# Optimization experiments

Hardware: AMD Instinct MI355X
Metric: run time of the kernel (lower is better)

The kernel has to match this reference:

```python
import jax, jax.numpy as jnp
import numpy as np

D_MODEL = 768
NUM_HEADS = 12
HEAD_DIM = D_MODEL // NUM_HEADS


def setup_inputs() -> dict:
    key = jax.random.key(0)
    ks = jax.random.split(key, 9)
    B, S = 2, 2048
    s = 1.0 / np.sqrt(D_MODEL)
    x = jax.random.normal(ks[0], (B, S, D_MODEL), dtype=jnp.float32)
    Wq = jax.random.normal(ks[1], (D_MODEL, D_MODEL), dtype=jnp.float32) * s
    Wk = jax.random.normal(ks[2], (D_MODEL, D_MODEL), dtype=jnp.float32) * s
    Wv = jax.random.normal(ks[3], (D_MODEL, D_MODEL), dtype=jnp.float32) * s
    Wo = jax.random.normal(ks[4], (D_MODEL, D_MODEL), dtype=jnp.float32) * s
    bq = jax.random.normal(ks[5], (D_MODEL,), dtype=jnp.float32) * 0.01
    bk = jax.random.normal(ks[6], (D_MODEL,), dtype=jnp.float32) * 0.01
    bv = jax.random.normal(ks[7], (D_MODEL,), dtype=jnp.float32) * 0.01
    bo = jax.random.normal(ks[8], (D_MODEL,), dtype=jnp.float32) * 0.01
    return {"x": x, "Wq": Wq, "bq": bq, "Wk": Wk, "bk": bk,
            "Wv": Wv, "bv": bv, "Wo": Wo, "bo": bo}


def reference(x, Wq, bq, Wk, bk, Wv, bv, Wo, bo):
    B, S, _ = x.shape
    # projections; reshape to [B, H, S, Dh]
    def split_heads(t):
        return t.reshape(B, S, NUM_HEADS, HEAD_DIM).transpose(0, 2, 1, 3)
    q = split_heads(x @ Wq + bq)
    k = split_heads(x @ Wk + bk)
    v = split_heads(x @ Wv + bv)
    scale = 1.0 / np.sqrt(HEAD_DIM)
    scores = jnp.einsum("bhqd,bhkd->bhqk", q, k) * scale  # [B,H,S,S]
    attn = jax.nn.softmax(scores, axis=-1)
    # dropout p=0.0 (eval) -> identity
    ctx = jnp.einsum("bhqk,bhkd->bhqd", attn, v)
    ctx = ctx.transpose(0, 2, 1, 3).reshape(B, S, D_MODEL)
    return ctx @ Wo + bo
```

## Files before the change

### kernel.cpp

```cpp
#include <hip/hip_runtime.h>
#include <hip/hip_bf16.h>
#include <hip/hip_fp16.h>

#define D_MODEL 768
#define NHEADS  12
#define HD      64
#define BATCH   2
#define SEQ     2048
#define NTOK    (BATCH*SEQ)
#define NX      ((size_t)NTOK * D_MODEL)
#define NW      ((size_t)D_MODEL * D_MODEL)
#define NBH     (BATCH*NHEADS)
#define SC_LOG2 0.18033688f

typedef __attribute__((ext_vector_type(8))) short    short8;
typedef __attribute__((ext_vector_type(8))) _Float16 half8;
typedef __attribute__((ext_vector_type(2))) __fp16   fp16x2;
typedef __attribute__((ext_vector_type(4))) float    f32x4;

__device__ __forceinline__ float bf2f(short s) {
    union { unsigned u; float f; } c;
    c.u = ((unsigned)(unsigned short)s) << 16;
    return c.f;
}
__device__ __forceinline__ short f2bf(float f) {
    __hip_bfloat16 h = __float2bfloat16(f);
    return *(short*)&h;
}

#ifdef __has_builtin
#if __has_builtin(__builtin_amdgcn_global_load_lds)
#define HAS_GLD 1
#endif
#if __has_builtin(__builtin_amdgcn_exp2f)
#define EXP2(x) __builtin_amdgcn_exp2f(x)
#else
#define EXP2(x) exp2f(x)
#endif
#if __has_builtin(__builtin_amdgcn_cvt_pkrtz)
#define HAS_PKRTZ 1
#endif
#else
#define EXP2(x) exp2f(x)
#endif
#ifdef HAS_GLD
#define GLD16(gp, lp) __builtin_amdgcn_global_load_lds( \
    (const __attribute__((address_space(1))) void*)(gp), \
    (__attribute__((address_space(3))) void*)(lp), 16, 0, 0)
#endif

#ifdef HAS_PKRTZ
#define PKF16(a, b) __builtin_amdgcn_cvt_pkrtz((a), (b))
#else
#define PKF16(a, b) ((fp16x2){ (__fp16)(a), (__fp16)(b) })
#endif

__global__ __launch_bounds__(256) void fused_conv(
        const void* __restrict__ xin,
        const void* __restrict__ w0, const void* __restrict__ w1,
        const void* __restrict__ w2, const void* __restrict__ w3,
        const void* __restrict__ b0, const void* __restrict__ b1,
        const void* __restrict__ b2, const void* __restrict__ b3,
        short* __restrict__ xc, short* __restrict__ wt,
        short* __restrict__ bc, int* __restrict__ flag)
{
    __shared__ int red[256];
    __shared__ float T[64][65];
    const int tid = threadIdx.x;
    const int F = blockIdx.x;

    {
        const short* xs = (const short*)xin;
        int maxe = 0;
#pragma unroll
        for (int u = 0; u < 16; ++u) {
            int e = ((unsigned short)xs[tid * 16 + u] >> 7) & 0xFF;
            maxe = max(maxe, e);
        }
        red[tid] = maxe;
        __syncthreads();
        for (int s = 128; s > 0; s >>= 1) {
            if (tid < s) red[tid] = max(red[tid], red[tid + s]);
            __syncthreads();
        }
    }
    const bool isf = (red[0] > 140);

    if (F < 3072) {
        const int i = F * 256 + tid;
        if (isf) {
            float4 f = ((const float4*)xin)[i];
            short4 o = { f2bf(f.x), f2bf(f.y), f2bf(f.z), f2bf(f.w) };
            ((short4*)xc)[i] = o;
        } else {
            ((short4*)xc)[i] = ((const short4*)xin)[i];
        }
    } else if (F < 3648) {
        const int G = F - 3072;
        const int z = G / 144, rr = G % 144;
        const int k0 = (rr % 12) * 64, n0 = (rr / 12) * 64;
        const void* src = (z == 0) ? w0 : (z == 1) ? w1 : (z == 2) ? w2 : w3;
        const float sc = (z == 0) ? SC_LOG2 : 1.0f;
        const int la = tid & 15, lb = tid >> 4;
#pragma unroll
        for (int u = 0; u < 4; ++u) {
            const int kr = (lb & 3) + 4 * u + 16 * (lb >> 2);
            if (isf) {
                float4 f = *(const float4*)((const float*)src + (size_t)(k0 + kr) * D_MODEL + n0 + la * 4);
                T[kr][la*4+0] = f.x; T[kr][la*4+1] = f.y; T[kr][la*4+2] = f.z; T[kr][la*4+3] = f.w;
            } else {
                short4 s = *(const short4*)((const short*)src + (size_t)(k0 + kr) * D_MODEL + n0 + la * 4);
                T[kr][la*4+0] = bf2f(s.x); T[kr][la*4+1] = bf2f(s.y);
                T[kr][la*4+2] = bf2f(s.z); T[kr][la*4+3] = bf2f(s.w);
            }
        }
        __syncthreads();
#pragma unroll
        for (int u = 0; u < 4; ++u) {
            const int nr = (lb & 3) + 4 * u + 16 * (lb >> 2);
            short4 o = { f2bf(T[la*4+0][nr] * sc), f2bf(T[la*4+1][nr] * sc),
                         f2bf(T[la*4+2][nr] * sc), f2bf(T[la*4+3][nr] * sc) };
            *(short4*)(wt + (size_t)z * NW + (size_t)(n0 + nr) * D_MODEL + k0 + la * 4) = o;
        }
    } else {
        if (tid == 0) *flag = isf ? 1 : 0;
        const void* srcs[4] = { b0, b1, b2, b3 };
        for (int z = 0; z < 4; ++z) {
            const float sc = (z == 0) ? SC_LOG2 : 1.0f;
            for (int i = tid; i < D_MODEL; i += 256) {
                float v = isf ? ((const float*)srcs[z])[i] : bf2f(((const short*)srcs[z])[i]);
                bc[z * D_MODEL + i] = f2bf(v * sc);
            }
        }
    }
}

__global__ __launch_bounds__(256) void qkv_gemm(const short* __restrict__ X,
                                                const short* __restrict__ Wt,
                                                const short* __restrict__ bias,
                                                short* __restrict__ qb,
                                                short* __restrict__ kb,
                                                _Float16* __restrict__ Vt)
{
    __shared__ __align__(16) char shbuf[24576];
    short* Als = (short*)shbuf;
    short* Bls = (short*)(shbuf + 8192);
    _Float16* T = (_Float16*)shbuf;

    const int tid = threadIdx.x;
    const int wave = tid >> 6, lane = tid & 63;
    const int quad = lane >> 4, l16 = lane & 15;
    const int wm = wave & 1, wn = wave >> 1;
    const int m0 = blockIdx.x * 64;
    const int ng = blockIdx.y * 128;

    f32x4 acc[2][4];
#pragma unroll
    for (int nt = 0; nt < 4; ++nt) {
        const float bv = bf2f(bias[ng + wn*64 + nt*16 + l16]);
#pragma unroll
        for (int mt = 0; mt < 2; ++mt) acc[mt][nt] = (f32x4){bv, bv, bv, bv};
    }

    const int row = tid >> 2, ch = (tid & 3) * 8;
#ifdef HAS_GLD
#define QSTAGE(buf, k0) do { \
        GLD16(X  + (size_t)(m0 + row)      * D_MODEL + (k0) + ch, &Als[(buf)*2048 + tid*8]); \
        GLD16(Wt + (size_t)(ng + row)      * D_MODEL + (k0) + ch, &Bls[(buf)*4096 + tid*8]); \
        GLD16(Wt + (size_t)(ng + 64 + row) * D_MODEL + (k0) + ch, &Bls[(buf)*4096 + 2048 + tid*8]); \
    } while (0)
#else
#define QSTAGE(buf, k0) do { \
        short8 r0 = *(const short8*)(X  + (size_t)(m0 + row)      * D_MODEL + (k0) + ch); \
        short8 r2 = *(const short8*)(Wt + (size_t)(ng + row)      * D_MODEL + (k0) + ch); \
        short8 r3 = *(const short8*)(Wt + (size_t)(ng + 64 + row) * D_MODEL + (k0) + ch); \
        *(short8*)&Als[(buf)*2048 + tid*8] = r0; \
        *(short8*)&Bls[(buf)*4096 + tid*8] = r2; \
        *(short8*)&Bls[(buf)*4096 + 2048 + tid*8] = r3; \
    } while (0)
#endif

    QSTAGE(0, 0);
    __syncthreads();

    for (int ks = 0; ks < 24; ++ks) {
        const int cur = ks & 1;
        if (ks + 1 < 24) QSTAGE(cur ^ 1, (ks + 1) * 32);

        short8 a[2], b[4];
#pragma unroll
        for (int mt = 0; mt < 2; ++mt)
            a[mt] = *(const short8*)&Als[cur*2048 + (wm*32 + mt*16 + l16) * 32 + quad*8];
#pragma unroll
        for (int nt = 0; nt < 4; ++nt)
            b[nt] = *(const short8*)&Bls[cur*4096 + (wn*64 + nt*16 + l16) * 32 + quad*8];
#pragma unroll
        for (int mt = 0; mt < 2; ++mt)
#pragma unroll
        for (int nt = 0; nt < 4; ++nt)
            acc[mt][nt] = __builtin_amdgcn_mfma_f32_16x16x32_bf16(a[mt], b[nt], acc[mt][nt], 0, 0, 0);

        __syncthreads();
    }
#undef QSTAGE

    const int seg = blockIdx.y / 6;
    if (seg < 2) {
        short* out = seg ? kb : qb;
        const int nl = ng - seg * 768;
#pragma unroll
        for (int mt = 0; mt < 2; ++mt)
#pragma unroll
        for (int nt = 0; nt < 4; ++nt) {
            const int n = nl + wn*64 + nt*16 + l16;
#pragma unroll
            for (int r = 0; r < 4; ++r) {
                const int m = m0 + wm*32 + mt*16 + quad*4 + r;
                out[(size_t)m * D_MODEL + n] = f2bf(acc[mt][nt][r]);
            }
        }
    } else {
        const int batch = m0 >> 11, tokb = m0 & (SEQ - 1);
#pragma unroll
        for (int nt = 0; nt < 4; ++nt) {
            const int dim_l = wn*64 + nt*16 + l16;
#pragma unroll
            for (int mt = 0; mt < 2; ++mt) {
                const int tok_l = wm*32 + mt*16 + quad*4;
                union { _Float16 h4[4]; int2 v; } u;
#pragma unroll
                for (int r = 0; r < 4; ++r) u.h4[r] = (_Float16)acc[mt][nt][r];
                *(int2*)&T[dim_l * 72 + tok_l] = u.v;
            }
        }
        __syncthreads();
#pragma unroll
        for (int u = 0; u < 4; ++u) {
            const int slot = tid + u * 256;
            const int drow = slot >> 3, chk = slot & 7;
            int4 val = *(const int4*)&T[drow * 72 + chk * 8];
            const int dim_g = ng - 1536 + drow;
            const int h = dim_g >> 6, d = dim_g & 63;
            *(int4*)(Vt + ((size_t)(batch * NHEADS + h) * HD + d) * SEQ + tokb + chk*8) = val;
        }
    }
}

__global__ __launch_bounds__(256) void out_gemm(const short* __restrict__ X,
                                                const short* __restrict__ Wt,
                                                const short* __restrict__ bias,
                                                void* __restrict__ outv,
                                                const int* __restrict__ flag)
{
    __shared__ short Als[2][2048];
    __shared__ short Bls[2][2048];

    const int tid = threadIdx.x;
    const int wave = tid >> 6, lane = tid & 63;
    const int quad = lane >> 4, l16 = lane & 15;
    const int m0 = blockIdx.x * 64;
    const int n0 = blockIdx.y * 64;

    f32x4 acc[4];
#pragma unroll
    for (int nt = 0; nt < 4; ++nt) {
        const float bv = bf2f(bias[n0 + nt*16 + l16]);
        acc[nt] = (f32x4){bv, bv, bv, bv};
    }

    const int row = tid >> 2, ch = (tid & 3) * 8;
#ifdef HAS_GLD
#define OSTAGE(buf, k0) do { \
        GLD16(X  + (size_t)(m0 + row) * D_MODEL + (k0) + ch, &Als[buf][tid*8]); \
        GLD16(Wt + (size_t)(n0 + row) * D_MODEL + (k0) + ch, &Bls[buf][tid*8]); \
    } while (0)
#else
#define OSTAGE(buf, k0) do { \
        short8 r0 = *(const short8*)(X  + (size_t)(m0 + row) * D_MODEL + (k0) + ch); \
        short8 r1 = *(const short8*)(Wt + (size_t)(n0 + row) * D_MODEL + (k0) + ch); \
        *(short8*)&Als[buf][tid*8] = r0; \
        *(short8*)&Bls[buf][tid*8] = r1; \
    } while (0)
#endif

    OSTAGE(0, 0);
    __syncthreads();

    for (int ks = 0; ks < 24; ++ks) {
        const int cur = ks & 1;
        if (ks + 1 < 24) OSTAGE(cur ^ 1, (ks + 1) * 32);

        short8 a = *(const short8*)&Als[cur][(wave*16 + l16) * 32 + quad*8];
#pragma unroll
        for (int nt = 0; nt < 4; ++nt) {
            short8 b = *(const short8*)&Bls[cur][(nt*16 + l16) * 32 + quad*8];
            acc[nt] = __builtin_amdgcn_mfma_f32_16x16x32_bf16(a, b, acc[nt], 0, 0, 0);
        }
        __syncthreads();
    }
#undef OSTAGE

    const bool outf32 = (*flag != 0);
#pragma unroll
    for (int nt = 0; nt < 4; ++nt) {
        const int n = n0 + nt*16 + l16;
#pragma unroll
        for (int r = 0; r < 4; ++r) {
            const int m = m0 + wave*16 + quad*4 + r;
            const size_t idx = (size_t)m * D_MODEL + n;
            if (outf32) ((float*)outv)[idx] = acc[nt][r];
            else        ((short*)outv)[idx] = f2bf(acc[nt][r]);
        }
    }
}

__global__ __launch_bounds__(256, 6) void attn_mfma(const short* __restrict__ q,
                                                    const short* __restrict__ k,
                                                    const _Float16* __restrict__ Vt,
                                                    _Float16* __restrict__ Op,
                                                    float* __restrict__ mlp)
{
    __shared__ short    Kls[2][2048];
    __shared__ _Float16 Vls[3][2048];
    __shared__ _Float16 Pls[4][512];

    const int tid  = threadIdx.x;
    const int wave = tid >> 6, lane = tid & 63;
    const int quad = lane >> 4, l16 = lane & 15;

    const int F = blockIdx.x;
    const int xcd = F & 7, slot = F >> 3;
    const int bh = xcd * 3 + (slot >> 6);
    const int rem = slot & 63;
    const int q0 = (rem >> 1) * 64;
    const int sp = rem & 1;
    const int kb0 = sp * (SEQ / 2);
    const int b = bh / NHEADS, h = bh % NHEADS;
    const size_t bS = (size_t)b * SEQ;
    const int myq = q0 + wave * 16 + l16;

    short8 qf[2];
#pragma unroll
    for (int k0h = 0; k0h < 2; ++k0h)
        qf[k0h] = *(const short8*)(q + (bS + myq) * D_MODEL + h*HD + k0h*32 + quad*8);

    half8 ones;
#pragma unroll
    for (int j = 0; j < 8; ++j) ones[j] = (_Float16)1.0f;

    const int cK = tid >> 5, keyK = tid & 31;
    const int cV = tid >> 6, dimV = tid & 63;
    const short*    kgp = k  + (bS + kb0 + keyK) * D_MODEL + h*HD + cK*8;
    const _Float16* vgp = Vt + ((size_t)bh * HD + dimV) * SEQ + kb0 + cV*8;

#ifdef HAS_GLD
#define STAGE_K(buf, j0) GLD16(kgp + (size_t)(j0) * D_MODEL, &Kls[buf][tid*8])
#define STAGE_V(buf, j0) GLD16(vgp + (j0),                   &Vls[buf][tid*8])
#else
#define STAGE_K(buf, j0) do { \
        short8 a_ = *(const short8*)(kgp + (size_t)(j0) * D_MODEL); \
        *(short8*)&Kls[buf][tid*8] = a_; } while (0)
#define STAGE_V(buf, j0) do { \
        half8 c_ = *(const half8*)(vgp + (j0)); \
        *(half8*)&Vls[buf][tid*8] = c_; } while (0)
#endif

    float m_ = -1e30f;
    f32x4 lacc = (f32x4){0.f, 0.f, 0.f, 0.f};
    f32x4 o[4];
#pragma unroll
    for (int t = 0; t < 4; ++t) o[t] = (f32x4){0.f, 0.f, 0.f, 0.f};

    f32x4 sA[2], sB[2];

#define NT (SEQ / 2 / 32)

#define QK(S, KB) do { \
    S[0] = (f32x4){0.f,0.f,0.f,0.f}; S[1] = (f32x4){0.f,0.f,0.f,0.f}; \
    __builtin_amdgcn_s_setprio(1); \
    _Pragma("unroll") \
    for (int k0h = 0; k0h < 2; ++k0h) \
    _Pragma("unroll") \
    for (int t = 0; t < 2; ++t) { \
        short8 kf = *(const short8*)&Kls[KB][(k0h*4 + quad)*256 + (t*16 + l16)*8]; \
        S[t] = __builtin_amdgcn_mfma_f32_16x16x32_bf16(kf, qf[k0h], S[t], 0, 0, 0); \
    } \
    __builtin_amdgcn_s_setprio(0); \
} while (0)

#define BODY(JT, SCUR, SNXT) do { \
    if ((JT) + 2 < NT) { \
        STAGE_K(((JT) + 2) & 1, ((JT) + 2) * 32); \
        STAGE_V(((JT) + 2) % 3, ((JT) + 2) * 32); \
    } \
    if ((JT) + 1 < NT) QK(SNXT, ((JT) + 1) & 1); \
    { \
         \
        float mx = SCUR[0][0]; \
        _Pragma("unroll") \
        for (int t = 0; t < 2; ++t) \
        _Pragma("unroll") \
        for (int r = 0; r < 4; ++r) mx = fmaxf(mx, SCUR[t][r]); \
        if (__any(mx > m_ + 8.f)) { \
            _Pragma("unroll") \
            for (int d = 1; d < 64; d <<= 1) mx = fmaxf(mx, __shfl_xor(mx, d)); \
            const float mn = fmaxf(m_, mx); \
            const float al = EXP2(m_ - mn); \
            _Pragma("unroll") \
            for (int t = 0; t < 4; ++t) { \
                o[t][0] *= al; o[t][1] *= al; o[t][2] *= al; o[t][3] *= al; \
            } \
            lacc[0] *= al; \
            m_ = mn; \
        } \
         \
        _Pragma("unroll") \
        for (int t = 0; t < 2; ++t) { \
            union { fp16x2 h2[2]; int2 v; } u4; \
            u4.h2[0] = PKF16(EXP2(SCUR[t][0] - m_), EXP2(SCUR[t][1] - m_)); \
            u4.h2[1] = PKF16(EXP2(SCUR[t][2] - m_), EXP2(SCUR[t][3] - m_)); \
            const int c = 2*t + (quad >> 1); \
            *(int2*)&Pls[wave][c*128 + l16*8 + (quad & 1)*4] = u4.v; \
        } \
         \
        const int vb = (JT) % 3; \
        half8 pf = *(half8*)&Pls[wave][quad*128 + l16*8]; \
        __builtin_amdgcn_s_setprio(1); \
        lacc = __builtin_amdgcn_mfma_f32_16x16x32_f16(ones, pf, lacc, 0, 0, 0); \
        _Pragma("unroll") \
        for (int t = 0; t < 4; ++t) { \
            half8 vf = *(const half8*)&Vls[vb][quad*512 + (t*16 + l16)*8]; \
            o[t] = __builtin_amdgcn_mfma_f32_16x16x32_f16(vf, pf, o[t], 0, 0, 0); \
        } \
        __builtin_amdgcn_s_setprio(0); \
    } \
    __syncthreads(); \
} while (0)

    STAGE_K(0, 0); STAGE_V(0, 0);
    __syncthreads();
    STAGE_K(1, 32); STAGE_V(1, 32);
    QK(sA, 0);
    __syncthreads();

    for (int jt = 0; jt < NT; jt += 2) {
        BODY(jt,     sA, sB);
        BODY(jt + 1, sB, sA);
    }

    const float inv = 1.0f / lacc[0];
    const size_t prow = ((size_t)sp * (NBH * SEQ) + (size_t)bh * SEQ + myq);
    _Float16* orow = Op + prow * HD;
#pragma unroll
    for (int t = 0; t < 4; ++t) {
        union { _Float16 h4[4]; int2 v; } u4;
#pragma unroll
        for (int r = 0; r < 4; ++r) u4.h4[r] = (_Float16)(o[t][r] * inv);
        *(int2*)(orow + t*16 + quad*4) = u4.v;
    }
    if (quad == 0) {
        float2 mlv; mlv.x = m_; mlv.y = lacc[0];
        *(float2*)&mlp[prow * 2] = mlv;
    }
#undef BODY
#undef QK
#undef NT
#undef STAGE_K
#undef STAGE_V
}

__global__ __launch_bounds__(256) void attn_combine(const _Float16* __restrict__ Op,
                                                    const float* __restrict__ mlp,
                                                    short* __restrict__ ctx)
{
    const int gid = blockIdx.x * 256 + threadIdx.x;
    const int r = gid >> 3, seg = gid & 7;
    const float2 a  = *(const float2*)&mlp[(size_t)r * 2];
    const float2 c2 = *(const float2*)&mlp[((size_t)(NBH * SEQ) + r) * 2];
    const float M  = fmaxf(a.x, c2.x);
    const float w1 = EXP2(a.x - M) * a.y;
    const float w2 = EXP2(c2.x - M) * c2.y;
    const float inv = 1.0f / (w1 + w2);
    const half8 o1 = *(const half8*)&Op[(size_t)r * HD + seg * 8];
    const half8 o2 = *(const half8*)&Op[(size_t)(NBH * SEQ) * HD + (size_t)r * HD + seg * 8];
    union { short s[8]; int4 v; } u;
#pragma unroll
    for (int j = 0; j < 8; ++j)
        u.s[j] = f2bf((w1 * (float)o1[j] + w2 * (float)o2[j]) * inv);
    const int bh = r >> 11, qq = r & (SEQ - 1);
    const int bb = bh / NHEADS, hh = bh % NHEADS;
    *(int4*)&ctx[((size_t)(bb * SEQ + qq)) * D_MODEL + hh * HD + seg * 8] = u.v;
}

extern "C" void kernel_launch(void* const* d_in, const int* in_sizes, int n_in,
                              void* d_out, int out_size, void* d_ws, size_t ws_size,
                              hipStream_t stream)
{
    int* flag = (int*)d_ws;
    short* xc = (short*)((char*)d_ws + 64);
    short* Wt = xc + NX;
    short* bc = Wt + 4 * NW;
    short* qb = bc + 4 * D_MODEL;
    short* kb = qb + NX;
    _Float16* Vt = (_Float16*)(kb + NX);
    short* cb = (short*)(Vt + NX);
    _Float16* Op = (_Float16*)(cb + NX);
    float* mlp = (float*)(Op + (size_t)2 * NBH * SEQ * HD);

    fused_conv<<<3649, 256, 0, stream>>>(d_in[0],
                                         d_in[1], d_in[3], d_in[5], d_in[7],
                                         d_in[2], d_in[4], d_in[6], d_in[8],
                                         xc, Wt, bc, flag);

    qkv_gemm<<<dim3(NTOK/64, 2304/128), 256, 0, stream>>>(xc, Wt, bc, qb, kb, Vt);

    attn_mfma<<<1536, 256, 0, stream>>>(qb, kb, Vt, Op, mlp);

    attn_combine<<<1536, 256, 0, stream>>>(Op, mlp, cb);

    out_gemm<<<dim3(NTOK/64, D_MODEL/64), 256, 0, stream>>>(cb, Wt + 3*NW, bc + 3*D_MODEL, d_out, flag);
}
```

Before: 189.8 us.

## Enlarge attention tiles to 32 queries per wave and 64-key blocks

Result: slower. 195.9 us (+3.2%).

```diff
diff --git a/kernel.cpp b/kernel.cpp
--- a/kernel.cpp
+++ b/kernel.cpp
@@ -314,15 +314,15 @@
     }
 }
 
-__global__ __launch_bounds__(256, 6) void attn_mfma(const short* __restrict__ q,
+__global__ __launch_bounds__(256, 3) void attn_mfma(const short* __restrict__ q,
                                                     const short* __restrict__ k,
                                                     const _Float16* __restrict__ Vt,
                                                     _Float16* __restrict__ Op,
                                                     float* __restrict__ mlp)
 {
-    __shared__ short    Kls[2][2048];
-    __shared__ _Float16 Vls[3][2048];
-    __shared__ _Float16 Pls[4][512];
+    __shared__ __align__(16) short    Kls[2][4096];
+    __shared__ __align__(16) _Float16 Vls[2][4096];
+    __shared__ __align__(16) _Float16 Pls[4][2048];
 
     const int tid  = threadIdx.x;
     const int wave = tid >> 6, lane = tid & 63;
@@ -330,107 +330,135 @@
 
     const int F = blockIdx.x;
     const int xcd = F & 7, slot = F >> 3;
-    const int bh = xcd * 3 + (slot >> 6);
-    const int rem = slot & 63;
-    const int q0 = (rem >> 1) * 64;
+    const int bh = xcd * 3 + (slot >> 5);
+    const int rem = slot & 31;
+    const int q0 = (rem >> 1) * 128;
     const int sp = rem & 1;
     const int kb0 = sp * (SEQ / 2);
     const int b = bh / NHEADS, h = bh % NHEADS;
     const size_t bS = (size_t)b * SEQ;
-    const int myq = q0 + wave * 16 + l16;
-
-    short8 qf[2];
+
+    short8 qf[2][2];
+#pragma unroll
+    for (int col = 0; col < 2; ++col)
 #pragma unroll
     for (int k0h = 0; k0h < 2; ++k0h)
-        qf[k0h] = *(const short8*)(q + (bS + myq) * D_MODEL + h*HD + k0h*32 + quad*8);
+        qf[col][k0h] = *(const short8*)(q + (bS + q0 + wave*32 + col*16 + l16) * D_MODEL
+                                          + h*HD + k0h*32 + quad*8);
 
     half8 ones;
 #pragma unroll
     for (int j = 0; j < 8; ++j) ones[j] = (_Float16)1.0f;
 
-    const int cK = tid >> 5, keyK = tid & 31;
-    const int cV = tid >> 6, dimV = tid & 63;
-    const short*    kgp = k  + (bS + kb0 + keyK) * D_MODEL + h*HD + cK*8;
-    const _Float16* vgp = Vt + ((size_t)bh * HD + dimV) * SEQ + kb0 + cV*8;
+    const int cK0 = tid >> 6,       keyK0 = tid & 63;
+    const int cK1 = (tid + 256) >> 6, keyK1 = tid & 63;
+    const short* kgp0 = k + (bS + kb0 + keyK0) * D_MODEL + h*HD + cK0*8;
+    const short* kgp1 = k + (bS + kb0 + keyK1) * D_MODEL + h*HD + cK1*8;
+    const _Float16* vgp0 = Vt + ((size_t)bh * HD + keyK0) * SEQ + kb0 + cK0*8;
+    const _Float16* vgp1 = Vt + ((size_t)bh * HD + keyK1) * SEQ + kb0 + cK1*8;
 
 #ifdef HAS_GLD
-#define STAGE_K(buf, j0) GLD16(kgp + (size_t)(j0) * D_MODEL, &Kls[buf][tid*8])
-#define STAGE_V(buf, j0) GLD16(vgp + (j0),                   &Vls[buf][tid*8])
+#define STAGE_K(buf, j0) do { \
+        GLD16(kgp0 + (size_t)(j0) * D_MODEL, &Kls[buf][tid*8]); \
+        GLD16(kgp1 + (size_t)(j0) * D_MODEL, &Kls[buf][(tid+256)*8]); \
+    } while (0)
+#define STAGE_V(buf, j0) do { \
+        GLD16(vgp0 + (j0), &Vls[buf][tid*8]); \
+        GLD16(vgp1 + (j0), &Vls[buf][(tid+256)*8]); \
+    } while (0)
 #else
 #define STAGE_K(buf, j0) do { \
-        short8 a_ = *(const short8*)(kgp + (size_t)(j0) * D_MODEL); \
-        *(short8*)&Kls[buf][tid*8] = a_; } while (0)
+        short8 a_ = *(const short8*)(kgp0 + (size_t)(j0) * D_MODEL); \
+        short8 b_ = *(const short8*)(kgp1 + (size_t)(j0) * D_MODEL); \
+        *(short8*)&Kls[buf][tid*8] = a_;  *(short8*)&Kls[buf][(tid+256)*8] = b_; \
+    } while (0)
 #define STAGE_V(buf, j0) do { \
-        half8 c_ = *(const half8*)(vgp + (j0)); \
-        *(half8*)&Vls[buf][tid*8] = c_; } while (0)
+        half8 c_ = *(const half8*)(vgp0 + (j0)); \
+        half8 d_ = *(const half8*)(vgp1 + (j0)); \
+        *(half8*)&Vls[buf][tid*8] = c_;  *(half8*)&Vls[buf][(tid+256)*8] = d_; \
+    } while (0)
 #endif
 
     float m_ = -1e30f;
-    f32x4 lacc = (f32x4){0.f, 0.f, 0.f, 0.f};
-    f32x4 o[4];
-#pragma unroll
-    for (int t = 0; t < 4; ++t) o[t] = (f32x4){0.f, 0.f, 0.f, 0.f};
-
-    f32x4 sA[2], sB[2];
-
-#define NT (SEQ / 2 / 32)
+    f32x4 laccA = (f32x4){0.f,0.f,0.f,0.f}, laccB = (f32x4){0.f,0.f,0.f,0.f};
+    f32x4 o[4][2];
+#pragma unroll
+    for (int t = 0; t < 4; ++t) { o[t][0] = (f32x4){0.f,0.f,0.f,0.f}; o[t][1] = (f32x4){0.f,0.f,0.f,0.f}; }
+
+    f32x4 sA[4][2], sB[4][2];
+
+#define NT (SEQ / 2 / 64)
 
 #define QK(S, KB) do { \
-    S[0] = (f32x4){0.f,0.f,0.f,0.f}; S[1] = (f32x4){0.f,0.f,0.f,0.f}; \
+    _Pragma("unroll") \
+    for (int t = 0; t < 4; ++t) { S[t][0] = (f32x4){0.f,0.f,0.f,0.f}; S[t][1] = (f32x4){0.f,0.f,0.f,0.f}; } \
     __builtin_amdgcn_s_setprio(1); \
     _Pragma("unroll") \
     for (int k0h = 0; k0h < 2; ++k0h) \
     _Pragma("unroll") \
-    for (int t = 0; t < 2; ++t) { \
-        short8 kf = *(const short8*)&Kls[KB][(k0h*4 + quad)*256 + (t*16 + l16)*8]; \
-        S[t] = __builtin_amdgcn_mfma_f32_16x16x32_bf16(kf, qf[k0h], S[t], 0, 0, 0); \
+    for (int t = 0; t < 4; ++t) { \
+        short8 kf = *(const short8*)&Kls[KB][(k0h*4 + quad)*512 + (t*16 + l16)*8]; \
+        S[t][0] = __builtin_amdgcn_mfma_f32_16x16x32_bf16(kf, qf[0][k0h], S[t][0], 0, 0, 0); \
+        S[t][1] = __builtin_amdgcn_mfma_f32_16x16x32_bf16(kf, qf[1][k0h], S[t][1], 0, 0, 0); \
     } \
     __builtin_amdgcn_s_setprio(0); \
 } while (0)
 
 #define BODY(JT, SCUR, SNXT) do { \
-    if ((JT) + 2 < NT) { \
-        STAGE_K(((JT) + 2) & 1, ((JT) + 2) * 32); \
-        STAGE_V(((JT) + 2) % 3, ((JT) + 2) * 32); \
+    if ((JT) + 2 < NT) STAGE_K(((JT) + 2) & 1, ((JT) + 2) * 64); \
+    if ((JT) + 1 < NT) { \
+        STAGE_V(((JT) + 1) & 1, ((JT) + 1) * 64); \
+        QK(SNXT, ((JT) + 1) & 1); \
     } \
-    if ((JT) + 1 < NT) QK(SNXT, ((JT) + 1) & 1); \
     { \
          \
-        float mx = SCUR[0][0]; \
+        float mx = SCUR[0][0][0]; \
         _Pragma("unroll") \
-        for (int t = 0; t < 2; ++t) \
+        for (int t = 0; t < 4; ++t) \
         _Pragma("unroll") \
-        for (int r = 0; r < 4; ++r) mx = fmaxf(mx, SCUR[t][r]); \
+        for (int c = 0; c < 2; ++c) \
+        _Pragma("unroll") \
+        for (int r = 0; r < 4; ++r) mx = fmaxf(mx, SCUR[t][c][r]); \
         if (__any(mx > m_ + 8.f)) { \
             _Pragma("unroll") \
             for (int d = 1; d < 64; d <<= 1) mx = fmaxf(mx, __shfl_xor(mx, d)); \
             const float mn = fmaxf(m_, mx); \
             const float al = EXP2(m_ - mn); \
             _Pragma("unroll") \
-            for (int t = 0; t < 4; ++t) { \
-                o[t][0] *= al; o[t][1] *= al; o[t][2] *= al; o[t][3] *= al; \
+            for (int t = 0; t < 4; ++t) \
+            _Pragma("unroll") \
+            for (int c = 0; c < 2; ++c) { \
+                o[t][c][0] *= al; o[t][c][1] *= al; o[t][c][2] *= al; o[t][c][3] *= al; \
             } \
-            lacc[0] *= al; \
+            laccA[0] *= al; laccB[0] *= al; \
             m_ = mn; \
         } \
          \
         _Pragma("unroll") \
-        for (int t = 0; t < 2; ++t) { \
+        for (int t = 0; t < 4; ++t) \
+        _Pragma("unroll") \
+        for (int c = 0; c < 2; ++c) { \
             union { fp16x2 h2[2]; int2 v; } u4; \
-            u4.h2[0] = PKF16(EXP2(SCUR[t][0] - m_), EXP2(SCUR[t][1] - m_)); \
-            u4.h2[1] = PKF16(EXP2(SCUR[t][2] - m_), EXP2(SCUR[t][3] - m_)); \
-            const int c = 2*t + (quad >> 1); \
-            *(int2*)&Pls[wave][c*128 + l16*8 + (quad & 1)*4] = u4.v; \
+            u4.h2[0] = PKF16(EXP2(SCUR[t][c][0] - m_), EXP2(SCUR[t][c][1] - m_)); \
+            u4.h2[1] = PKF16(EXP2(SCUR[t][c][2] - m_), EXP2(SCUR[t][c][3] - m_)); \
+            const int kc = 2*t + (quad >> 1); \
+            *(int2*)&Pls[wave][c*1024 + kc*128 + l16*8 + (quad & 1)*4] = u4.v; \
         } \
          \
-        const int vb = (JT) % 3; \
-        half8 pf = *(half8*)&Pls[wave][quad*128 + l16*8]; \
+        const int vb = (JT) & 1; \
         __builtin_amdgcn_s_setprio(1); \
-        lacc = __builtin_amdgcn_mfma_f32_16x16x32_f16(ones, pf, lacc, 0, 0, 0); \
         _Pragma("unroll") \
-        for (int t = 0; t < 4; ++t) { \
-            half8 vf = *(const half8*)&Vls[vb][quad*512 + (t*16 + l16)*8]; \
-            o[t] = __builtin_amdgcn_mfma_f32_16x16x32_f16(vf, pf, o[t], 0, 0, 0); \
+        for (int k0h = 0; k0h < 2; ++k0h) { \
+            half8 pf0 = *(half8*)&Pls[wave][(k0h*4 + quad)*128 + l16*8]; \
+            half8 pf1 = *(half8*)&Pls[wave][1024 + (k0h*4 + quad)*128 + l16*8]; \
+            laccA = __builtin_amdgcn_mfma_f32_16x16x32_f16(ones, pf0, laccA, 0, 0, 0); \
+            laccB = __builtin_amdgcn_mfma_f32_16x16x32_f16(ones, pf1, laccB, 0, 0, 0); \
+            _Pragma("unroll") \
+            for (int t = 0; t < 4; ++t) { \
+                half8 vf = *(const half8*)&Vls[vb][(k0h*4 + quad)*512 + (t*16 + l16)*8]; \
+                o[t][0] = __builtin_amdgcn_mfma_f32_16x16x32_f16(vf, pf0, o[t][0], 0, 0, 0); \
+                o[t][1] = __builtin_amdgcn_mfma_f32_16x16x32_f16(vf, pf1, o[t][1], 0, 0, 0); \
+            } \
         } \
         __builtin_amdgcn_s_setprio(0); \
     } \
@@ -439,7 +467,7 @@
 
     STAGE_K(0, 0); STAGE_V(0, 0);
     __syncthreads();
-    STAGE_K(1, 32); STAGE_V(1, 32);
+    STAGE_K(1, 64);
     QK(sA, 0);
     __syncthreads();
 
@@ -448,19 +476,24 @@
         BODY(jt + 1, sB, sA);
     }
 
-    const float inv = 1.0f / lacc[0];
-    const size_t prow = ((size_t)sp * (NBH * SEQ) + (size_t)bh * SEQ + myq);
-    _Float16* orow = Op + prow * HD;
-#pragma unroll
-    for (int t = 0; t < 4; ++t) {
-        union { _Float16 h4[4]; int2 v; } u4;
-#pragma unroll
-        for (int r = 0; r < 4; ++r) u4.h4[r] = (_Float16)(o[t][r] * inv);
-        *(int2*)(orow + t*16 + quad*4) = u4.v;
-    }
-    if (quad == 0) {
-        float2 mlv; mlv.x = m_; mlv.y = lacc[0];
-        *(float2*)&mlp[prow * 2] = mlv;
+#pragma unroll
+    for (int col = 0; col < 2; ++col) {
+        const f32x4 la = col ? laccB : laccA;
+        const float inv = 1.0f / la[0];
+        const int myq = q0 + wave*32 + col*16 + l16;
+        const size_t prow = ((size_t)sp * (NBH * SEQ) + (size_t)bh * SEQ + myq);
+        _Float16* orow = Op + prow * HD;
+#pragma unroll
+        for (int t = 0; t < 4; ++t) {
+            union { _Float16 h4[4]; int2 v; } u4;
+#pragma unroll
+            for (int r = 0; r < 4; ++r) u4.h4[r] = (_Float16)(o[t][col][r] * inv);
+            *(int2*)(orow + t*16 + quad*4) = u4.v;
+        }
+        if (quad == 0) {
+            float2 mlv; mlv.x = m_; mlv.y = la[0];
+            *(float2*)&mlp[prow * 2] = mlv;
+        }
     }
 #undef BODY
 #undef QK
@@ -514,7 +547,7 @@
 
     qkv_gemm<<<dim3(NTOK/64, 2304/128), 256, 0, stream>>>(xc, Wt, bc, qb, kb, Vt);
 
-    attn_mfma<<<1536, 256, 0, stream>>>(qb, kb, Vt, Op, mlp);
+    attn_mfma<<<768, 256, 0, stream>>>(qb, kb, Vt, Op, mlp);
 
     attn_combine<<<1536, 256, 0, stream>>>(Op, mlp, cb);
 
```
